# Performance work log

Measured on AMD Instinct MI355X. Metric: run time of the kernel, lower is better.

Reference implementation:

```python
import jax, jax.numpy as jnp
import numpy as np

D_MODEL, D_INNER, D_STATE, D_CONV = 1024, 2048, 16, 4
LN_EPS = 1e-5


def setup_inputs() -> dict:
    key = jax.random.key(0)
    ks = jax.random.split(key, 8)
    B, T = 2, 1024
    s = 0.02
    A = jnp.broadcast_to(jnp.arange(1, D_STATE + 1, dtype=jnp.float32), (D_INNER, D_STATE))
    return {
        "x": jax.random.normal(ks[0], (B, T, D_MODEL), jnp.float32),
        "ln_gamma": jnp.ones((D_MODEL,), jnp.float32),
        "ln_beta": jnp.zeros((D_MODEL,), jnp.float32),
        "W_in": jax.random.normal(ks[1], (2 * D_INNER, D_MODEL), jnp.float32) * s,
        "conv_w": jax.random.normal(ks[2], (D_INNER, D_CONV), jnp.float32) * s,
        "conv_b": jnp.zeros((D_INNER,), jnp.float32),
        "W_x": jax.random.normal(ks[3], (2 * D_STATE + 1, D_INNER), jnp.float32) * s,
        "w_dt": jax.random.normal(ks[4], (D_INNER, 1), jnp.float32) * s,
        "b_dt": jnp.zeros((D_INNER,), jnp.float32),
        "A_log": jnp.log(A),
        "D_param": jnp.ones((D_INNER,), jnp.float32),
        "W_out": jax.random.normal(ks[5], (D_MODEL, D_INNER), jnp.float32) * s,
    }


def _mamba_forward(x, ln_gamma, ln_beta, W_in, conv_w, conv_b, W_x, w_dt, b_dt, A_log, D_param, W_out):
    residual = x
    B, T, _ = x.shape
    # LayerNorm
    mu = x.mean(-1, keepdims=True)
    var = ((x - mu) ** 2).mean(-1, keepdims=True)
    xn = (x - mu) / jnp.sqrt(var + LN_EPS) * ln_gamma + ln_beta
    # in_proj -> split into x branch and gate z
    xz = xn @ W_in.T                       # [B,T,2*d_inner]
    xb, z = jnp.split(xz, 2, axis=-1)
    # depthwise causal conv1d (torch pad=d_conv-1, truncated to T == left pad)
    xp = jnp.pad(xb, ((0, 0), (D_CONV - 1, 0), (0, 0)))
    xc = conv_b + sum(xp[:, k:k + T, :] * conv_w[:, k] for k in range(D_CONV))
    xc = jax.nn.silu(xc)                   # [B,T,d_inner]
    # ssm parameter projections
    ssm_p = xc @ W_x.T                     # [B,T,2*d_state+1]
    dt_raw = ssm_p[..., :1]
    Bp = ssm_p[..., 1:1 + D_STATE]
    Cp = ssm_p[..., 1 + D_STATE:]
    dt = jax.nn.softplus(dt_raw @ w_dt.T + b_dt)   # [B,T,d_inner]
    A = -jnp.exp(A_log)                    # [d_inner,d_state]

    def step(h, inp):
        dt_t, x_t, B_t, C_t = inp          # [B,d], [B,d], [B,n], [B,n]
        A_bar = jnp.exp(dt_t[:, :, None] * A[None])          # [B,d,n]
        h = A_bar * h + (dt_t * x_t)[:, :, None] * B_t[:, None, :]
        y_t = jnp.einsum('bdn,bn->bd', h, C_t)
        return h, y_t

    h0 = jnp.zeros((B, D_INNER, D_STATE), x.dtype)
    xs = (jnp.swapaxes(dt, 0, 1), jnp.swapaxes(xc, 0, 1),
          jnp.swapaxes(Bp, 0, 1), jnp.swapaxes(Cp, 0, 1))
    _, ys = jax.lax.scan(step, h0, xs)     # ys: [T,B,d_inner]
    y = jnp.swapaxes(ys, 0, 1)
    y = y + D_param * xc
    y = y * jax.nn.silu(z)
    return residual + y @ W_out.T


def reference(x, ln_gamma, ln_beta, W_in, conv_w, conv_b, W_x, w_dt, b_dt, A_log, D_param, W_out):
    return _mamba_forward(x, ln_gamma, ln_beta, W_in, conv_w, conv_b, W_x, w_dt, b_dt, A_log, D_param, W_out)
```

## Files before the change

kernel.cpp:

```cpp
#include <hip/hip_runtime.h>
#include <hip/hip_bf16.h>

#define DM 1024
#define DI 2048
#define DS 16
#define DC 4
#define BB 2
#define TT 1024
#define MM (BB*TT)
#define CCH 32
#define LCH 32
#define PR 8

typedef unsigned short u16;
typedef __attribute__((ext_vector_type(8))) short bf16x8;
typedef __attribute__((ext_vector_type(4))) float f32x4;

#if __has_builtin(__builtin_amdgcn_exp2f)
#define EXP2F(x) __builtin_amdgcn_exp2f(x)
#else
#define EXP2F(x) exp2f(x)
#endif
#define L2E 1.44269504f

__device__ __forceinline__ float bu2f(u16 u) {
    union { unsigned int i; float f; } w; w.i = ((unsigned int)u) << 16; return w.f;
}
__device__ __forceinline__ u16 f2bu(float f) {
    union { float f; unsigned int u; } w; w.f = f;
    unsigned int r = w.u + 0x7fffu + ((w.u >> 16) & 1u);
    return (u16)(r >> 16);
}
__device__ __forceinline__ float upk(const uint4& v, int e) {
    unsigned int u;
    switch (e >> 1) { case 0: u = v.x; break; case 1: u = v.y; break;
                      case 2: u = v.z; break; default: u = v.w; }
    union { unsigned int i; float f; } w;
    w.i = (e & 1) ? (u & 0xffff0000u) : (u << 16);
    return w.f;
}

#define F2B_BLOCKS 6210
__global__ __launch_bounds__(256) void prep_kernel(const float* __restrict__ x,
                                                   const float* __restrict__ gamma,
                                                   const float* __restrict__ beta,
                                                   u16* __restrict__ xn,
                                                   const float* __restrict__ Wi,
                                                   u16* __restrict__ Wi_b,
                                                   const float* __restrict__ Wo,
                                                   u16* __restrict__ Wo_b,
                                                   const float* __restrict__ Wx,
                                                   u16* __restrict__ Wx_b) {
    const int tid = threadIdx.x;
    if (blockIdx.x >= MM) {
        const int n4W  = 2 * DI * DM / 4;
        const int n4Wo = DM * DI / 4;
        int i = (blockIdx.x - MM) * 256 + tid;
        const float* in; u16* out;
        if (i < n4W) { in = Wi; out = Wi_b; }
        else if (i < n4W + n4Wo) { in = Wo; out = Wo_b; i -= n4W; }
        else { in = Wx; out = Wx_b; i -= n4W + n4Wo; }
        float4 v = reinterpret_cast<const float4*>(in)[i];
        ushort4 o;
        o.x = f2bu(v.x); o.y = f2bu(v.y); o.z = f2bu(v.z); o.w = f2bu(v.w);
        reinterpret_cast<ushort4*>(out)[i] = o;
        return;
    }
    __shared__ float sbuf[8];
    const int row = blockIdx.x;
    float4 v = reinterpret_cast<const float4*>(x + (size_t)row * DM)[tid];

    float s = v.x + v.y + v.z + v.w;
    #pragma unroll
    for (int off = 32; off; off >>= 1) s += __shfl_down(s, off);
    if ((tid & 63) == 0) sbuf[tid >> 6] = s;
    __syncthreads();
    float mu = (sbuf[0] + sbuf[1] + sbuf[2] + sbuf[3]) * (1.0f / DM);
    __syncthreads();

    float d0 = v.x - mu, d1 = v.y - mu, d2 = v.z - mu, d3 = v.w - mu;
    float q = d0*d0 + d1*d1 + d2*d2 + d3*d3;
    #pragma unroll
    for (int off = 32; off; off >>= 1) q += __shfl_down(q, off);
    if ((tid & 63) == 0) sbuf[tid >> 6] = q;
    __syncthreads();
    float var = (sbuf[0] + sbuf[1] + sbuf[2] + sbuf[3]) * (1.0f / DM);
    float rstd = rsqrtf(var + 1e-5f);

    float4 g = reinterpret_cast<const float4*>(gamma)[tid];
    float4 b = reinterpret_cast<const float4*>(beta)[tid];
    ushort4 o;
    o.x = f2bu(d0 * rstd * g.x + b.x);
    o.y = f2bu(d1 * rstd * g.y + b.y);
    o.z = f2bu(d2 * rstd * g.z + b.z);
    o.w = f2bu(d3 * rstd * g.w + b.w);
    reinterpret_cast<ushort4*>(xn + (size_t)row * DM)[tid] = o;
}

__device__ __forceinline__ void gl_lds(const u16* g, u16* lds) {
    __builtin_amdgcn_global_load_lds((const __attribute__((address_space(1))) void*)g,
                                     (__attribute__((address_space(3))) void*)lds,
                                     16, 0, 0);
}

__global__ __launch_bounds__(256) void gemm1_mfma(const u16* __restrict__ A,
                                                  const u16* __restrict__ B,
                                                  u16* __restrict__ C,
                                                  int M, int N, int K) {
    __shared__ u16 As[2][2][128 * 32];
    __shared__ u16 Bs[2][2][128 * 32];
    const int tid  = threadIdx.x;
    const int lane = tid & 63;
    const int w    = tid >> 6;
    const int wm   = (w >> 1) * 64, wn = (w & 1) * 64;
    const int m0   = blockIdx.y * 128, n0 = blockIdx.x * 128;

    const int srow = tid >> 2;
    const int sk   = (((tid & 3) ^ ((srow >> 1) & 3)) * 8);
    const u16* aP0 = A + (size_t)(m0 + srow) * K + sk;
    const u16* aP1 = aP0 + (size_t)64 * K;
    const u16* bP0 = B + (size_t)(n0 + srow) * K + sk;
    const u16* bP1 = bP0 + (size_t)64 * K;
    const int ldst = tid * 8;

    const int fr = lane & 15, fq = (lane >> 4) * 8;

    #pragma unroll
    for (int kh = 0; kh < 2; kh++) {
        gl_lds(aP0 + kh * 32, &As[0][kh][ldst]); gl_lds(aP1 + kh * 32, &As[0][kh][2048 + ldst]);
        gl_lds(bP0 + kh * 32, &Bs[0][kh][ldst]); gl_lds(bP1 + kh * 32, &Bs[0][kh][2048 + ldst]);
    }
    __syncthreads();

    const int iters = K >> 6;
    f32x4 acc[4][4] = {};
    for (int it = 0; it < iters; it++) {
        const int cur = it & 1;
        const int kn = (it + 1) << 6;
        if (kn < K) {
            const int nb = cur ^ 1;
            #pragma unroll
            for (int kh = 0; kh < 2; kh++) {
                gl_lds(aP0 + kn + kh * 32, &As[nb][kh][ldst]);
                gl_lds(aP1 + kn + kh * 32, &As[nb][kh][2048 + ldst]);
                gl_lds(bP0 + kn + kh * 32, &Bs[nb][kh][ldst]);
                gl_lds(bP1 + kn + kh * 32, &Bs[nb][kh][2048 + ldst]);
            }
        }
        #pragma unroll
        for (int kh = 0; kh < 2; kh++) {
            bf16x8 af[4], bf[4];
            #pragma unroll
            for (int i = 0; i < 4; i++) {
                const int ra = wm + i * 16 + fr;
                af[i] = *reinterpret_cast<const bf16x8*>(
                    &As[cur][kh][ra * 32 + (fq ^ (((ra >> 1) & 3) << 3))]);
            }
            #pragma unroll
            for (int j = 0; j < 4; j++) {
                const int rb = wn + j * 16 + fr;
                bf[j] = *reinterpret_cast<const bf16x8*>(
                    &Bs[cur][kh][rb * 32 + (fq ^ (((rb >> 1) & 3) << 3))]);
            }
            #pragma unroll
            for (int i = 0; i < 4; i++)
                #pragma unroll
                for (int j = 0; j < 4; j++)
                    acc[i][j] = __builtin_amdgcn_mfma_f32_16x16x32_bf16(af[i], bf[j], acc[i][j], 0, 0, 0);
        }
        __syncthreads();
    }

    const int erow = (lane >> 4) * 4, ecol = lane & 15;
    #pragma unroll
    for (int i = 0; i < 4; i++)
        #pragma unroll
        for (int j = 0; j < 4; j++) {
            const int col = n0 + wn + j * 16 + ecol;
            #pragma unroll
            for (int r = 0; r < 4; r++) {
                const int row = m0 + wm + i * 16 + erow + r;
                C[(size_t)row * N + col] = f2bu(acc[i][j][r]);
            }
        }
}

__global__ __launch_bounds__(256) void gemm2_mfma(const u16* __restrict__ A,
                                                  const u16* __restrict__ B,
                                                  float* __restrict__ C,
                                                  const float* __restrict__ resid,
                                                  int M, int N, int K) {
    __shared__ u16 As[2][4][64 * 32];
    __shared__ u16 Bs[2][4][64 * 32];
    const int tid  = threadIdx.x;
    const int lane = tid & 63;
    const int w    = tid >> 6;
    const int wm   = (w >> 1) * 32, wn = (w & 1) * 32;
    const int m0   = blockIdx.y * 64, n0 = blockIdx.x * 64;

    const int srow = tid >> 2;
    const int sk   = (((tid & 3) ^ ((srow >> 1) & 3)) * 8);
    const u16* aP = A + (size_t)(m0 + srow) * K + sk;
    const u16* bP = B + (size_t)(n0 + srow) * K + sk;
    const int ldst = tid * 8;

    const int fr = lane & 15, fq = (lane >> 4) * 8;

    #pragma unroll
    for (int kh = 0; kh < 4; kh++) {
        gl_lds(aP + kh * 32, &As[0][kh][ldst]);
        gl_lds(bP + kh * 32, &Bs[0][kh][ldst]);
    }
    __syncthreads();

    const int iters = K >> 7;
    f32x4 acc[2][2] = {};
    for (int it = 0; it < iters; it++) {
        const int cur = it & 1;
        const int kn = (it + 1) << 7;
        if (kn < K) {
            const int nb = cur ^ 1;
            #pragma unroll
            for (int kh = 0; kh < 4; kh++) {
                gl_lds(aP + kn + kh * 32, &As[nb][kh][ldst]);
                gl_lds(bP + kn + kh * 32, &Bs[nb][kh][ldst]);
            }
        }
        #pragma unroll
        for (int kh = 0; kh < 4; kh++) {
            bf16x8 af[2], bf[2];
            #pragma unroll
            for (int i = 0; i < 2; i++) {
                const int ra = wm + i * 16 + fr;
                af[i] = *reinterpret_cast<const bf16x8*>(
                    &As[cur][kh][ra * 32 + (fq ^ (((ra >> 1) & 3) << 3))]);
            }
            #pragma unroll
            for (int j = 0; j < 2; j++) {
                const int rb = wn + j * 16 + fr;
                bf[j] = *reinterpret_cast<const bf16x8*>(
                    &Bs[cur][kh][rb * 32 + (fq ^ (((rb >> 1) & 3) << 3))]);
            }
            #pragma unroll
            for (int i = 0; i < 2; i++)
                #pragma unroll
                for (int j = 0; j < 2; j++)
                    acc[i][j] = __builtin_amdgcn_mfma_f32_16x16x32_bf16(af[i], bf[j], acc[i][j], 0, 0, 0);
        }
        __syncthreads();
    }

    const int erow = (lane >> 4) * 4, ecol = lane & 15;
    #pragma unroll
    for (int i = 0; i < 2; i++)
        #pragma unroll
        for (int j = 0; j < 2; j++) {
            const int col = n0 + wn + j * 16 + ecol;
            #pragma unroll
            for (int r = 0; r < 4; r++) {
                const int row = m0 + wm + i * 16 + erow + r;
                C[(size_t)row * N + col] = acc[i][j][r] + resid[(size_t)row * N + col];
            }
        }
}

__global__ __launch_bounds__(256) void convproj_kernel(const u16* __restrict__ xz,
                                                       const float* __restrict__ cw,
                                                       const float* __restrict__ cb,
                                                       const u16* __restrict__ Wxb,
                                                       u16* __restrict__ xc,
                                                       float* __restrict__ ssm) {
    __shared__ u16 xs[64 * PR * 32];
    __shared__ float red[4][PR][48];
    const int tid  = threadIdx.x;
    const int row0 = blockIdx.x * PR;
    const int t0   = row0 & (TT - 1);
    const int d0   = tid * 8;

    float4 w4[8];
    #pragma unroll
    for (int e = 0; e < 8; e++) w4[e] = reinterpret_cast<const float4*>(cw)[d0 + e];
    float bias[8];
    *reinterpret_cast<float4*>(&bias[0]) = reinterpret_cast<const float4*>(cb + d0)[0];
    *reinterpret_cast<float4*>(&bias[4]) = reinterpret_cast<const float4*>(cb + d0)[1];

    uint4 pk[PR + 3];
    #pragma unroll
    for (int j = 0; j < PR + 3; j++) {
        const int tr = t0 - 3 + j;
        if (tr >= 0)
            pk[j] = *reinterpret_cast<const uint4*>(xz + (size_t)(row0 - 3 + j) * (2 * DI) + d0);
        else
            pk[j] = make_uint4(0, 0, 0, 0);
    }

    const int kt_w = tid >> 2;
    const int ko_w = (tid & 3) * 8;
    #pragma unroll
    for (int r = 0; r < PR; r++) {
        u16 ob[8];
        #pragma unroll
        for (int e = 0; e < 8; e++) {
            float a = bias[e]
                    + upk(pk[r],     e) * w4[e].x
                    + upk(pk[r + 1], e) * w4[e].y
                    + upk(pk[r + 2], e) * w4[e].z
                    + upk(pk[r + 3], e) * w4[e].w;
            float sv = a / (1.0f + __expf(-a));
            ob[e] = f2bu(sv);
        }
        uint4 o;
        o.x = (unsigned)ob[0] | ((unsigned)ob[1] << 16);
        o.y = (unsigned)ob[2] | ((unsigned)ob[3] << 16);
        o.z = (unsigned)ob[4] | ((unsigned)ob[5] << 16);
        o.w = (unsigned)ob[6] | ((unsigned)ob[7] << 16);
        *reinterpret_cast<uint4*>(xc + (size_t)(row0 + r) * DI + d0) = o;
        *reinterpret_cast<uint4*>(&xs[kt_w * (PR * 32) + r * 32 + ko_w]) = o;
    }
    __syncthreads();

    const int lane = tid & 63, w = tid >> 6;
    const int fr = lane & 15, fq = (lane >> 4) * 8;
    const int kt0 = w * 16;
    const u16* b0p = Wxb + (size_t)(fr)      * DI + fq;
    const u16* b1p = Wxb + (size_t)(16 + fr) * DI + fq;
    const u16* b2p = Wxb + (size_t)32        * DI + fq;

    f32x4 acc0 = {}, acc1 = {}, acc2 = {};
    bf16x8 a_c = *reinterpret_cast<const bf16x8*>(&xs[kt0 * (PR * 32) + (fr & 7) * 32 + fq]);
    bf16x8 b0c = *reinterpret_cast<const bf16x8*>(b0p + (size_t)kt0 * 32);
    bf16x8 b1c = *reinterpret_cast<const bf16x8*>(b1p + (size_t)kt0 * 32);
    bf16x8 b2c = *reinterpret_cast<const bf16x8*>(b2p + (size_t)kt0 * 32);
    #pragma unroll
    for (int i = 0; i < 16; i++) {
        bf16x8 a_n, b0n, b1n, b2n;
        if (i < 15) {
            const int ktn = kt0 + i + 1;
            a_n = *reinterpret_cast<const bf16x8*>(&xs[ktn * (PR * 32) + (fr & 7) * 32 + fq]);
            b0n = *reinterpret_cast<const bf16x8*>(b0p + (size_t)ktn * 32);
            b1n = *reinterpret_cast<const bf16x8*>(b1p + (size_t)ktn * 32);
            b2n = *reinterpret_cast<const bf16x8*>(b2p + (size_t)ktn * 32);
        }
        acc0 = __builtin_amdgcn_mfma_f32_16x16x32_bf16(a_c, b0c, acc0, 0, 0, 0);
        acc1 = __builtin_amdgcn_mfma_f32_16x16x32_bf16(a_c, b1c, acc1, 0, 0, 0);
        acc2 = __builtin_amdgcn_mfma_f32_16x16x32_bf16(a_c, b2c, acc2, 0, 0, 0);
        if (i < 15) { a_c = a_n; b0c = b0n; b1c = b1n; b2c = b2n; }
    }
    const int erow = (lane >> 4) * 4, ecol = lane & 15;
    if (erow < PR) {
        #pragma unroll
        for (int r = 0; r < 4; r++) {
            red[w][erow + r][0 * 16 + ecol] = acc0[r];
            red[w][erow + r][1 * 16 + ecol] = acc1[r];
            red[w][erow + r][2 * 16 + ecol] = acc2[r];
        }
    }
    __syncthreads();

    for (int idx = tid; idx < PR * 33; idx += 256) {
        const int rr = idx / 33, n = idx % 33;
        float s = red[0][rr][n] + red[1][rr][n] + red[2][rr][n] + red[3][rr][n];
        ssm[(size_t)(row0 + rr) * 33 + n] = s;
    }
}

__global__ __launch_bounds__(256) void scan_part1(const float* __restrict__ ssm,
                                                  const u16* __restrict__ xcy,
                                                  const float* __restrict__ w_dt,
                                                  const float* __restrict__ b_dt,
                                                  const float* __restrict__ A_log,
                                                  float* __restrict__ F,
                                                  float* __restrict__ Sdt) {
    __shared__ float sm[LCH * 33];
    __shared__ u16 xls[LCH * 256];
    const int tid = threadIdx.x;
    const int dt8 = blockIdx.x & 7;
    const int bc  = blockIdx.x >> 3;
    const int c   = bc & (CCH - 1);
    const int b   = bc >> 5;
    const int d   = dt8 * 256 + tid;

    const int base = ((b * TT) + c * LCH) * 33;
    for (int i = tid; i < LCH * 33; i += 256) sm[i] = ssm[base + i];
    const u16* xg = xcy + (size_t)(b * TT + c * LCH) * DI + dt8 * 256;
    for (int i = tid; i < LCH * 128; i += 256) {
        int t = i >> 7, dp = i & 127;
        unsigned int v = *reinterpret_cast<const unsigned int*>(xg + (size_t)t * DI + dp * 2);
        *reinterpret_cast<unsigned int*>(&xls[t * 256 + dp * 2]) = v;
    }
    __syncthreads();

    float A2[DS], h[DS];
    float4 al[4];
    #pragma unroll
    for (int i = 0; i < 4; i++)
        al[i] = reinterpret_cast<const float4*>(A_log + (size_t)d * DS)[i];
    #pragma unroll
    for (int i = 0; i < 4; i++) {
        A2[4*i+0] = -__expf(al[i].x) * L2E;
        A2[4*i+1] = -__expf(al[i].y) * L2E;
        A2[4*i+2] = -__expf(al[i].z) * L2E;
        A2[4*i+3] = -__expf(al[i].w) * L2E;
    }
    #pragma unroll
    for (int n = 0; n < DS; n++) h[n] = 0.f;
    const float wdt = w_dt[d], bdt = b_dt[d];
    float sdt = 0.f;

    for (int t = 0; t < LCH; t++) {
        const float* sp = &sm[t * 33];
        float pre = sp[0] * wdt + bdt;
        float dtv = (pre > 20.f) ? pre : __logf(1.f + __expf(pre));
        sdt += dtv;
        float xv = bu2f(xls[t * 256 + tid]);
        float u = dtv * xv;
        #pragma unroll
        for (int n = 0; n < DS; n++) h[n] = EXP2F(dtv * A2[n]) * h[n] + u * sp[1 + n];
    }
    const size_t fo = ((size_t)(b * CCH + c) * DI + d) * DS;
    #pragma unroll
    for (int n = 0; n < DS; n++) F[fo + n] = h[n];
    Sdt[(b * CCH + c) * DI + d] = sdt;
}

__global__ __launch_bounds__(256) void scan_part2(const float* __restrict__ ssm,
                                                  const u16* __restrict__ xz,
                                                  u16* __restrict__ xcy,
                                                  const float* __restrict__ w_dt,
                                                  const float* __restrict__ b_dt,
                                                  const float* __restrict__ A_log,
                                                  const float* __restrict__ Dp,
                                                  const float* __restrict__ F,
                                                  const float* __restrict__ Sdt) {
    __shared__ float sm[LCH * 33];
    __shared__ u16 xls[LCH * 256];
    const int tid = threadIdx.x;
    const int dt8 = blockIdx.x & 7;
    const int bc  = blockIdx.x >> 3;
    const int c   = bc & (CCH - 1);
    const int b   = bc >> 5;
    const int d   = dt8 * 256 + tid;

    const int base = ((b * TT) + c * LCH) * 33;
    for (int i = tid; i < LCH * 33; i += 256) sm[i] = ssm[base + i];
    const u16* xg = xcy + (size_t)(b * TT + c * LCH) * DI + dt8 * 256;
    for (int i = tid; i < LCH * 128; i += 256) {
        int t = i >> 7, dp = i & 127;
        unsigned int v = *reinterpret_cast<const unsigned int*>(xg + (size_t)t * DI + dp * 2);
        *reinterpret_cast<unsigned int*>(&xls[t * 256 + dp * 2]) = v;
    }
    __syncthreads();

    float A2[DS], h[DS];
    float4 al[4];
    #pragma unroll
    for (int i = 0; i < 4; i++)
        al[i] = reinterpret_cast<const float4*>(A_log + (size_t)d * DS)[i];
    #pragma unroll
    for (int i = 0; i < 4; i++) {
        A2[4*i+0] = -__expf(al[i].x) * L2E;
        A2[4*i+1] = -__expf(al[i].y) * L2E;
        A2[4*i+2] = -__expf(al[i].z) * L2E;
        A2[4*i+3] = -__expf(al[i].w) * L2E;
    }

    #pragma unroll
    for (int n = 0; n < DS; n++) h[n] = 0.f;
    for (int cc = 0; cc < c; cc++) {
        const float sdt = Sdt[(size_t)(b * CCH + cc) * DI + d];
        const float4* fp = reinterpret_cast<const float4*>(
            F + ((size_t)(b * CCH + cc) * DI + d) * DS);
        float fa[DS];
        #pragma unroll
        for (int i = 0; i < 4; i++) {
            float4 fv = fp[i];
            fa[4*i+0] = fv.x; fa[4*i+1] = fv.y; fa[4*i+2] = fv.z; fa[4*i+3] = fv.w;
        }
        #pragma unroll
        for (int n = 0; n < DS; n++) h[n] = EXP2F(sdt * A2[n]) * h[n] + fa[n];
    }

    const float wdt = w_dt[d], bdt = b_dt[d], Dv = Dp[d];

    for (int t = 0; t < LCH; t++) {
        const float* sp = &sm[t * 33];
        float pre = sp[0] * wdt + bdt;
        float dtv = (pre > 20.f) ? pre : __logf(1.f + __expf(pre));
        const size_t row = (size_t)(b * TT + c * LCH + t);
        float xv = bu2f(xls[t * 256 + tid]);
        float u = dtv * xv;
        float y = 0.f;
        #pragma unroll
        for (int n = 0; n < DS; n++) {
            h[n] = EXP2F(dtv * A2[n]) * h[n] + u * sp[1 + n];
            y += h[n] * sp[17 + n];
        }
        float z = bu2f(xz[row * (2 * DI) + DI + d]);
        float sz = z / (1.0f + __expf(-z));
        xcy[row * DI + d] = f2bu((y + Dv * xv) * sz);
    }
}

extern "C" void kernel_launch(void* const* d_in, const int* in_sizes, int n_in,
                              void* d_out, int out_size, void* d_ws, size_t ws_size,
                              hipStream_t stream) {
    int ix, ig, ib, iWin, icw, icb, iWx, iwdt, ibdt, iAl, iD, iWo;
    if (n_in >= 12 && in_sizes[0] == 32768) {
        iAl = 0; iD = 1; iWin = 2; iWo = 3; iWx = 4; ibdt = 5;
        icb = 6; icw = 7; ib = 8; ig = 9; iwdt = 10; ix = 11;
    } else if (n_in >= 12 && in_sizes[0] == 2097152 && in_sizes[1] == 2048 && in_sizes[2] == 32768) {
        iWo = 0; iD = 1; iAl = 2; ibdt = 3; iwdt = 4; iWx = 5;
        icb = 6; icw = 7; iWin = 8; ib = 9; ig = 10; ix = 11;
    } else {
        ix = 0; ig = 1; ib = 2; iWin = 3; icw = 4; icb = 5;
        iWx = 6; iwdt = 7; ibdt = 8; iAl = 9; iD = 10; iWo = 11;
    }

    const float* x       = (const float*)d_in[ix];
    const float* ln_g    = (const float*)d_in[ig];
    const float* ln_b    = (const float*)d_in[ib];
    const float* W_in    = (const float*)d_in[iWin];
    const float* conv_w  = (const float*)d_in[icw];
    const float* conv_b  = (const float*)d_in[icb];
    const float* W_x     = (const float*)d_in[iWx];
    const float* w_dt    = (const float*)d_in[iwdt];
    const float* b_dt    = (const float*)d_in[ibdt];
    const float* A_log   = (const float*)d_in[iAl];
    const float* D_param = (const float*)d_in[iD];
    const float* W_out   = (const float*)d_in[iWo];
    float* out = (float*)d_out;

    float* ssm  = (float*)d_ws;
    u16*   xn   = (u16*)(ssm + (size_t)MM * 33);
    u16*   xz   = xn + (size_t)MM * DM;
    u16*   xcy  = xz + (size_t)MM * 2 * DI;
    float* F    = (float*)(xcy + (size_t)MM * DI);
    float* Sdt  = F + (size_t)BB * CCH * DI * DS;
    u16*   Wi_b = (u16*)(Sdt + (size_t)BB * CCH * DI);
    u16*   Wo_b = Wi_b + (size_t)2 * DI * DM;
    u16*   Wx_b = Wo_b + (size_t)DM * DI;

    prep_kernel<<<MM + F2B_BLOCKS, 256, 0, stream>>>(x, ln_g, ln_b, xn, W_in, Wi_b,
                                                     W_out, Wo_b, W_x, Wx_b);

    gemm1_mfma<<<dim3(4096 / 128, MM / 128), 256, 0, stream>>>(xn, Wi_b, xz, MM, 2 * DI, DM);

    convproj_kernel<<<MM / PR, 256, 0, stream>>>(xz, conv_w, conv_b, Wx_b, xcy, ssm);

    scan_part1<<<BB * CCH * (DI / 256), 256, 0, stream>>>(ssm, xcy, w_dt, b_dt, A_log, F, Sdt);
    scan_part2<<<BB * CCH * (DI / 256), 256, 0, stream>>>(ssm, xz, xcy, w_dt, b_dt, A_log,
                                                          D_param, F, Sdt);

    gemm2_mfma<<<dim3(1024 / 64, MM / 64), 256, 0, stream>>>(xcy, Wo_b, out, x, MM, DM, DI);
}
```

Measured before the change: 210.5 us.

## Compute chunk-carry prefix once via last-block atomic; vectorize B/C smem reads

The inter-chunk state prefix was recomputed by every scan_part2 block, looping over all preceding chunks (quadratic work in chunk count). Now the last scan_part1 block for each (batch, d-slice) group, found with an atomic counter and threadfence, runs a single sequential prefix and overwrites F with each chunk's incoming state. scan_part2 then just loads its initial state. The smem row is padded to 36 floats so B and C can be read as float4. This adds a serialized tail on one block per group and depends on the counter being reset in prep_kernel on every call.

```diff
diff --git a/kernel.cpp b/kernel.cpp
--- a/kernel.cpp
+++ b/kernel.cpp
@@ -11,6 +11,7 @@
 #define CCH 32
 #define LCH 32
 #define PR 8
+#define SMW 36
 
 typedef unsigned short u16;
 typedef __attribute__((ext_vector_type(8))) short bf16x8;
@@ -50,8 +51,10 @@
                                                    const float* __restrict__ Wo,
                                                    u16* __restrict__ Wo_b,
                                                    const float* __restrict__ Wx,
-                                                   u16* __restrict__ Wx_b) {
+                                                   u16* __restrict__ Wx_b,
+                                                   int* __restrict__ cnt) {
     const int tid = threadIdx.x;
+    if (blockIdx.x == 0 && tid < BB * 8) cnt[tid] = 0;
     if (blockIdx.x >= MM) {
         const int n4W  = 2 * DI * DM / 4;
         const int n4Wo = DM * DI / 4;
@@ -370,8 +373,112 @@
                                                   const float* __restrict__ b_dt,
                                                   const float* __restrict__ A_log,
                                                   float* __restrict__ F,
-                                                  float* __restrict__ Sdt) {
-    __shared__ float sm[LCH * 33];
+                                                  float* __restrict__ Sdt,
+                                                  int* __restrict__ cnt) {
+    __shared__ float sm[LCH * SMW];
+    __shared__ u16 xls[LCH * 256];
+    __shared__ int lastFlag;
+    const int tid = threadIdx.x;
+    const int dt8 = blockIdx.x & 7;
+    const int bc  = blockIdx.x >> 3;
+    const int c   = bc & (CCH - 1);
+    const int b   = bc >> 5;
+    const int d   = dt8 * 256 + tid;
+
+    const int base = ((b * TT) + c * LCH) * 33;
+    for (int i = tid; i < LCH * 33; i += 256) {
+        int t = i / 33, j = i % 33;
+        sm[t * SMW + (j == 0 ? 0 : j + 3)] = ssm[base + i];
+    }
+    const u16* xg = xcy + (size_t)(b * TT + c * LCH) * DI + dt8 * 256;
+    for (int i = tid; i < LCH * 128; i += 256) {
+        int t = i >> 7, dp = i & 127;
+        unsigned int v = *reinterpret_cast<const unsigned int*>(xg + (size_t)t * DI + dp * 2);
+        *reinterpret_cast<unsigned int*>(&xls[t * 256 + dp * 2]) = v;
+    }
+    __syncthreads();
+
+    float A2[DS], h[DS];
+    float4 al[4];
+    #pragma unroll
+    for (int i = 0; i < 4; i++)
+        al[i] = reinterpret_cast<const float4*>(A_log + (size_t)d * DS)[i];
+    #pragma unroll
+    for (int i = 0; i < 4; i++) {
+        A2[4*i+0] = -__expf(al[i].x) * L2E;
+        A2[4*i+1] = -__expf(al[i].y) * L2E;
+        A2[4*i+2] = -__expf(al[i].z) * L2E;
+        A2[4*i+3] = -__expf(al[i].w) * L2E;
+    }
+    #pragma unroll
+    for (int n = 0; n < DS; n++) h[n] = 0.f;
+    const float wdt = w_dt[d], bdt = b_dt[d];
+    float sdt = 0.f;
+
+    for (int t = 0; t < LCH; t++) {
+        const float* sp = &sm[t * SMW];
+        float Bv[DS];
+        #pragma unroll
+        for (int i = 0; i < 4; i++) {
+            float4 bv = *reinterpret_cast<const float4*>(sp + 4 + 4 * i);
+            Bv[4*i+0] = bv.x; Bv[4*i+1] = bv.y; Bv[4*i+2] = bv.z; Bv[4*i+3] = bv.w;
+        }
+        float pre = sp[0] * wdt + bdt;
+        float dtv = (pre > 20.f) ? pre : __logf(1.f + __expf(pre));
+        sdt += dtv;
+        float xv = bu2f(xls[t * 256 + tid]);
+        float u = dtv * xv;
+        #pragma unroll
+        for (int n = 0; n < DS; n++) h[n] = EXP2F(dtv * A2[n]) * h[n] + u * Bv[n];
+    }
+    const size_t fo = ((size_t)(b * CCH + c) * DI + d) * DS;
+    #pragma unroll
+    for (int n = 0; n < DS; n++) F[fo + n] = h[n];
+    Sdt[(b * CCH + c) * DI + d] = sdt;
+
+    __threadfence();
+    if (tid == 0) {
+        int old = atomicAdd(&cnt[b * 8 + dt8], 1);
+        lastFlag = (old == CCH - 1);
+    }
+    __syncthreads();
+    if (lastFlag) {
+        __threadfence();
+        float h2[DS];
+        #pragma unroll
+        for (int n = 0; n < DS; n++) h2[n] = 0.f;
+        for (int cc = 0; cc < CCH; cc++) {
+            const size_t o = ((size_t)(b * CCH + cc) * DI + d) * DS;
+            float4 f0 = *reinterpret_cast<const float4*>(F + o);
+            float4 f1 = *reinterpret_cast<const float4*>(F + o + 4);
+            float4 f2 = *reinterpret_cast<const float4*>(F + o + 8);
+            float4 f3 = *reinterpret_cast<const float4*>(F + o + 12);
+            float sdtc = Sdt[(size_t)(b * CCH + cc) * DI + d];
+            float fa[DS] = { f0.x, f0.y, f0.z, f0.w, f1.x, f1.y, f1.z, f1.w,
+                             f2.x, f2.y, f2.z, f2.w, f3.x, f3.y, f3.z, f3.w };
+            float hc[DS];
+            #pragma unroll
+            for (int n = 0; n < DS; n++) {
+                hc[n] = h2[n];
+                h2[n] = EXP2F(sdtc * A2[n]) * h2[n] + fa[n];
+            }
+            *reinterpret_cast<float4*>(F + o)      = make_float4(hc[0], hc[1], hc[2], hc[3]);
+            *reinterpret_cast<float4*>(F + o + 4)  = make_float4(hc[4], hc[5], hc[6], hc[7]);
+            *reinterpret_cast<float4*>(F + o + 8)  = make_float4(hc[8], hc[9], hc[10], hc[11]);
+            *reinterpret_cast<float4*>(F + o + 12) = make_float4(hc[12], hc[13], hc[14], hc[15]);
+        }
+    }
+}
+
+__global__ __launch_bounds__(256) void scan_part2(const float* __restrict__ ssm,
+                                                  const u16* __restrict__ xz,
+                                                  u16* __restrict__ xcy,
+                                                  const float* __restrict__ w_dt,
+                                                  const float* __restrict__ b_dt,
+                                                  const float* __restrict__ A_log,
+                                                  const float* __restrict__ Dp,
+                                                  const float* __restrict__ Hin) {
+    __shared__ float sm[LCH * SMW];
     __shared__ u16 xls[LCH * 256];
     const int tid = threadIdx.x;
     const int dt8 = blockIdx.x & 7;
@@ -381,7 +488,10 @@
     const int d   = dt8 * 256 + tid;
 
     const int base = ((b * TT) + c * LCH) * 33;
-    for (int i = tid; i < LCH * 33; i += 256) sm[i] = ssm[base + i];
+    for (int i = tid; i < LCH * 33; i += 256) {
+        int t = i / 33, j = i % 33;
+        sm[t * SMW + (j == 0 ? 0 : j + 3)] = ssm[base + i];
+    }
     const u16* xg = xcy + (size_t)(b * TT + c * LCH) * DI + dt8 * 256;
     for (int i = tid; i < LCH * 128; i += 256) {
         int t = i >> 7, dp = i & 127;
@@ -402,88 +512,21 @@
         A2[4*i+2] = -__expf(al[i].z) * L2E;
         A2[4*i+3] = -__expf(al[i].w) * L2E;
     }
-    #pragma unroll
-    for (int n = 0; n < DS; n++) h[n] = 0.f;
-    const float wdt = w_dt[d], bdt = b_dt[d];
-    float sdt = 0.f;
+    const size_t ho = ((size_t)(b * CCH + c) * DI + d) * DS;
+    #pragma unroll
+    for (int n = 0; n < DS; n++) h[n] = Hin[ho + n];
+    const float wdt = w_dt[d], bdt = b_dt[d], Dv = Dp[d];
 
     for (int t = 0; t < LCH; t++) {
-        const float* sp = &sm[t * 33];
-        float pre = sp[0] * wdt + bdt;
-        float dtv = (pre > 20.f) ? pre : __logf(1.f + __expf(pre));
-        sdt += dtv;
-        float xv = bu2f(xls[t * 256 + tid]);
-        float u = dtv * xv;
-        #pragma unroll
-        for (int n = 0; n < DS; n++) h[n] = EXP2F(dtv * A2[n]) * h[n] + u * sp[1 + n];
-    }
-    const size_t fo = ((size_t)(b * CCH + c) * DI + d) * DS;
-    #pragma unroll
-    for (int n = 0; n < DS; n++) F[fo + n] = h[n];
-    Sdt[(b * CCH + c) * DI + d] = sdt;
-}
-
-__global__ __launch_bounds__(256) void scan_part2(const float* __restrict__ ssm,
-                                                  const u16* __restrict__ xz,
-                                                  u16* __restrict__ xcy,
-                                                  const float* __restrict__ w_dt,
-                                                  const float* __restrict__ b_dt,
-                                                  const float* __restrict__ A_log,
-                                                  const float* __restrict__ Dp,
-                                                  const float* __restrict__ F,
-                                                  const float* __restrict__ Sdt) {
-    __shared__ float sm[LCH * 33];
-    __shared__ u16 xls[LCH * 256];
-    const int tid = threadIdx.x;
-    const int dt8 = blockIdx.x & 7;
-    const int bc  = blockIdx.x >> 3;
-    const int c   = bc & (CCH - 1);
-    const int b   = bc >> 5;
-    const int d   = dt8 * 256 + tid;
-
-    const int base = ((b * TT) + c * LCH) * 33;
-    for (int i = tid; i < LCH * 33; i += 256) sm[i] = ssm[base + i];
-    const u16* xg = xcy + (size_t)(b * TT + c * LCH) * DI + dt8 * 256;
-    for (int i = tid; i < LCH * 128; i += 256) {
-        int t = i >> 7, dp = i & 127;
-        unsigned int v = *reinterpret_cast<const unsigned int*>(xg + (size_t)t * DI + dp * 2);
-        *reinterpret_cast<unsigned int*>(&xls[t * 256 + dp * 2]) = v;
-    }
-    __syncthreads();
-
-    float A2[DS], h[DS];
-    float4 al[4];
-    #pragma unroll
-    for (int i = 0; i < 4; i++)
-        al[i] = reinterpret_cast<const float4*>(A_log + (size_t)d * DS)[i];
-    #pragma unroll
-    for (int i = 0; i < 4; i++) {
-        A2[4*i+0] = -__expf(al[i].x) * L2E;
-        A2[4*i+1] = -__expf(al[i].y) * L2E;
-        A2[4*i+2] = -__expf(al[i].z) * L2E;
-        A2[4*i+3] = -__expf(al[i].w) * L2E;
-    }
-
-    #pragma unroll
-    for (int n = 0; n < DS; n++) h[n] = 0.f;
-    for (int cc = 0; cc < c; cc++) {
-        const float sdt = Sdt[(size_t)(b * CCH + cc) * DI + d];
-        const float4* fp = reinterpret_cast<const float4*>(
-            F + ((size_t)(b * CCH + cc) * DI + d) * DS);
-        float fa[DS];
+        const float* sp = &sm[t * SMW];
+        float Bv[DS], Cv[DS];
         #pragma unroll
         for (int i = 0; i < 4; i++) {
-            float4 fv = fp[i];
-            fa[4*i+0] = fv.x; fa[4*i+1] = fv.y; fa[4*i+2] = fv.z; fa[4*i+3] = fv.w;
-        }
-        #pragma unroll
-        for (int n = 0; n < DS; n++) h[n] = EXP2F(sdt * A2[n]) * h[n] + fa[n];
-    }
-
-    const float wdt = w_dt[d], bdt = b_dt[d], Dv = Dp[d];
-
-    for (int t = 0; t < LCH; t++) {
-        const float* sp = &sm[t * 33];
+            float4 bv = *reinterpret_cast<const float4*>(sp + 4 + 4 * i);
+            Bv[4*i+0] = bv.x; Bv[4*i+1] = bv.y; Bv[4*i+2] = bv.z; Bv[4*i+3] = bv.w;
+            float4 cv = *reinterpret_cast<const float4*>(sp + 20 + 4 * i);
+            Cv[4*i+0] = cv.x; Cv[4*i+1] = cv.y; Cv[4*i+2] = cv.z; Cv[4*i+3] = cv.w;
+        }
         float pre = sp[0] * wdt + bdt;
         float dtv = (pre > 20.f) ? pre : __logf(1.f + __expf(pre));
         const size_t row = (size_t)(b * TT + c * LCH + t);
@@ -492,8 +535,8 @@
         float y = 0.f;
         #pragma unroll
         for (int n = 0; n < DS; n++) {
-            h[n] = EXP2F(dtv * A2[n]) * h[n] + u * sp[1 + n];
-            y += h[n] * sp[17 + n];
+            h[n] = EXP2F(dtv * A2[n]) * h[n] + u * Bv[n];
+            y += h[n] * Cv[n];
         }
         float z = bu2f(xz[row * (2 * DI) + DI + d]);
         float sz = z / (1.0f + __expf(-z));
@@ -539,17 +582,19 @@
     u16*   Wi_b = (u16*)(Sdt + (size_t)BB * CCH * DI);
     u16*   Wo_b = Wi_b + (size_t)2 * DI * DM;
     u16*   Wx_b = Wo_b + (size_t)DM * DI;
+    int*   cnt  = (int*)(Wx_b + (size_t)33 * DI);
 
     prep_kernel<<<MM + F2B_BLOCKS, 256, 0, stream>>>(x, ln_g, ln_b, xn, W_in, Wi_b,
-                                                     W_out, Wo_b, W_x, Wx_b);
+                                                     W_out, Wo_b, W_x, Wx_b, cnt);
 
     gemm1_mfma<<<dim3(4096 / 128, MM / 128), 256, 0, stream>>>(xn, Wi_b, xz, MM, 2 * DI, DM);
 
     convproj_kernel<<<MM / PR, 256, 0, stream>>>(xz, conv_w, conv_b, Wx_b, xcy, ssm);
 
-    scan_part1<<<BB * CCH * (DI / 256), 256, 0, stream>>>(ssm, xcy, w_dt, b_dt, A_log, F, Sdt);
+    scan_part1<<<BB * CCH * (DI / 256), 256, 0, stream>>>(ssm, xcy, w_dt, b_dt, A_log,
+                                                          F, Sdt, cnt);
     scan_part2<<<BB * CCH * (DI / 256), 256, 0, stream>>>(ssm, xz, xcy, w_dt, b_dt, A_log,
-                                                          D_param, F, Sdt);
+                                                          D_param, F);
 
     gemm2_mfma<<<dim3(1024 / 64, MM / 64), 256, 0, stream>>>(xcy, Wo_b, out, x, MM, DM, DI);
 }
```

Result: slower. 304.2 us (+44.5%).
